# Performance work log

Measured on AMD Instinct MI355X. Metric: run time of the kernel, lower is better.

## Reference

```python
import jax, jax.numpy as jnp
import numpy as np

N, E = 20000, 320000
IN, OUT, H1, H2 = 256, 32, 8, 1
NEG_SLOPE = 0.2


def _gatv2(x, src, dst, Wsrc, bsrc, Wdst, bdst, attn, Wres, bres, heads, dout):
    n = x.shape[0]
    fs = (x @ Wsrc + bsrc).reshape(n, heads, dout)   # (N,H,D)
    fd = (x @ Wdst + bdst).reshape(n, heads, dout)   # (N,H,D)
    # GATv2: leaky_relu BEFORE the attention dot product
    e = jax.nn.leaky_relu(fs[src] + fd[dst], NEG_SLOPE)      # (E,H,D)
    logits = jnp.einsum('ehd,hd->eh', e, attn)               # (E,H)
    # edge softmax over destination-node segments
    m = jax.ops.segment_max(logits, dst, num_segments=n)     # (N,H)
    ex = jnp.exp(logits - m[dst])
    s = jax.ops.segment_sum(ex, dst, num_segments=n)         # (N,H)
    alpha = ex / s[dst]                                      # (E,H)
    msg = alpha[:, :, None] * fs[src]                        # (E,H,D)
    out = jax.ops.segment_sum(msg, dst, num_segments=n)      # (N,H,D)
    res = (x @ Wres + bres).reshape(n, heads, dout)          # residual (dims differ -> Linear)
    return out + res


def setup_inputs() -> dict:
    key = jax.random.key(0)
    ks = jax.random.split(key, 16)
    sc = lambda fin: 1.0 / np.sqrt(fin)
    d = {}
    d['x'] = jax.random.normal(ks[0], (N, IN), jnp.float32)
    d['src'] = jax.random.randint(ks[1], (E,), 0, N, jnp.int32)
    d['dst'] = jax.random.randint(ks[2], (E,), 0, N, jnp.int32)
    # layer 1: IN -> OUT*H1
    d['Wsrc1'] = jax.random.normal(ks[3], (IN, OUT * H1), jnp.float32) * sc(IN)
    d['bsrc1'] = jnp.zeros((OUT * H1,), jnp.float32)
    d['Wdst1'] = jax.random.normal(ks[4], (IN, OUT * H1), jnp.float32) * sc(IN)
    d['bdst1'] = jnp.zeros((OUT * H1,), jnp.float32)
    d['attn1'] = jax.random.normal(ks[5], (H1, OUT), jnp.float32) * sc(OUT)
    d['Wres1'] = jax.random.normal(ks[6], (IN, OUT * H1), jnp.float32) * sc(IN)
    d['bres1'] = jnp.zeros((OUT * H1,), jnp.float32)
    # layer 2: OUT*H1 -> OUT, 1 head
    D2 = OUT * H1
    d['Wsrc2'] = jax.random.normal(ks[7], (D2, OUT * H2), jnp.float32) * sc(D2)
    d['bsrc2'] = jnp.zeros((OUT * H2,), jnp.float32)
    d['Wdst2'] = jax.random.normal(ks[8], (D2, OUT * H2), jnp.float32) * sc(D2)
    d['bdst2'] = jnp.zeros((OUT * H2,), jnp.float32)
    d['attn2'] = jax.random.normal(ks[9], (H2, OUT), jnp.float32) * sc(OUT)
    d['Wres2'] = jax.random.normal(ks[10], (D2, OUT * H2), jnp.float32) * sc(D2)
    d['bres2'] = jnp.zeros((OUT * H2,), jnp.float32)
    return d


def reference(x, src, dst,
              Wsrc1, bsrc1, Wdst1, bdst1, attn1, Wres1, bres1,
              Wsrc2, bsrc2, Wdst2, bdst2, attn2, Wres2, bres2):
    y = _gatv2(x, src, dst, Wsrc1, bsrc1, Wdst1, bdst1, attn1, Wres1, bres1, H1, OUT)
    y = jax.nn.relu(y)                       # (N, 8, OUT)
    y = y.reshape(x.shape[0], -1)            # (N, 8*OUT)
    y = _gatv2(y, src, dst, Wsrc2, bsrc2, Wdst2, bdst2, attn2, Wres2, bres2, H2, OUT)
    return y                                  # (N, 1, OUT)
```

## Files before the change

kernel.cpp:

```cpp
#include <hip/hip_runtime.h>
#include <hip/hip_bf16.h>

#define N_NODES 20000
#define N_PAD   20096
#define N_EDGES 320000
#define D_IN    256
#define NEG     0.2f
#define MAXDEG  64

typedef __attribute__((ext_vector_type(8))) short short8;
typedef __attribute__((ext_vector_type(4))) float f32x4;
typedef __attribute__((ext_vector_type(4))) unsigned short u16x4;

__device__ __forceinline__ unsigned short f2b(float f) {
    unsigned int u = __float_as_uint(f);
    unsigned int r = (u + 0x7FFFu + ((u >> 16) & 1u)) >> 16;
    return (unsigned short)r;
}
__device__ __forceinline__ float b2f(unsigned short u) {
    union { unsigned int i; float f; } v;
    v.i = ((unsigned int)u) << 16;
    return v.f;
}

__device__ __forceinline__ void gload16(const void* g, void* l) {
    __builtin_amdgcn_global_load_lds((const __attribute__((address_space(1))) void*)g,
                                     (__attribute__((address_space(3))) void*)l, 16, 0, 0);
}

#define PB1 2512
#define PB2 3280
#define PB3 3376
#define PB4 3455
#define PREP_BLOCKS 3503
__global__ __launch_bounds__(256) void k_prep(
    const float* __restrict__ x, unsigned short* __restrict__ xb,
    const float* __restrict__ Ws1, const float* __restrict__ Wd1, const float* __restrict__ Wr1,
    unsigned short* __restrict__ wt,
    const float* __restrict__ Ws2, const float* __restrict__ Wd2, const float* __restrict__ Wr2,
    unsigned short* __restrict__ wt2,
    int* __restrict__ cnt, unsigned short* __restrict__ yb)
{
    int bid = blockIdx.x, tid = threadIdx.x;
    if (bid < PB1) {
        int i = bid * 256 + tid;
        int row = i >> 5, c8 = (i & 31) * 8;
        short8 v = {0, 0, 0, 0, 0, 0, 0, 0};
        if (row < N_NODES) {
            float4 a = *reinterpret_cast<const float4*>(x + (size_t)row * 256 + c8);
            float4 b = *reinterpret_cast<const float4*>(x + (size_t)row * 256 + c8 + 4);
            v[0] = (short)f2b(a.x); v[1] = (short)f2b(a.y); v[2] = (short)f2b(a.z); v[3] = (short)f2b(a.w);
            v[4] = (short)f2b(b.x); v[5] = (short)f2b(b.y); v[6] = (short)f2b(b.z); v[7] = (short)f2b(b.w);
        }
        *reinterpret_cast<short8*>(xb + (size_t)row * 256 + c8) = v;
    } else if (bid < PB2) {
        int n = bid - PB1, k = tid;
        const float* W = (n < 256) ? Ws1 : ((n < 512) ? Wd1 : Wr1);
        int c = n & 255;
        wt[(size_t)n * 256 + k] = f2b(W[(size_t)k * 256 + c]);
    } else if (bid < PB3) {
        int n = bid - PB2, k = tid;
        const float* W = (n < 32) ? Ws2 : ((n < 64) ? Wd2 : Wr2);
        int c = n & 31;
        wt2[(size_t)n * 256 + (k ^ ((n & 7) << 3))] = f2b(W[(size_t)k * 32 + c]);
    } else if (bid < PB4) {
        int idx = (bid - PB3) * 256 + tid;
        if (idx < N_NODES) cnt[idx] = 0;
    } else {
        int j = (bid - PB4) * 256 + tid;
        ((unsigned int*)(yb + (size_t)N_NODES * 256))[j] = 0u;
    }
}

#define GEMM1_BLOCKS 942
#define BUCKET_BLOCKS 1250
__global__ __launch_bounds__(256) void k_gemm_l1_mfma(
    const unsigned short* __restrict__ xb,
    const unsigned short* __restrict__ wt,
    const float* __restrict__ bs, const float* __restrict__ bd, const float* __restrict__ br,
    unsigned short* __restrict__ fs, unsigned short* __restrict__ fd, unsigned short* __restrict__ res,
    const int* __restrict__ src, const int* __restrict__ dst,
    int* __restrict__ cnt, int* __restrict__ colp)
{
    __shared__ __align__(16) unsigned short SH[2 * 128 * 64];
    int t = threadIdx.x;
    int bid = blockIdx.x;

    if (bid >= GEMM1_BLOCKS) {
        int e = (bid - GEMM1_BLOCKS) * 256 + t;
        if (e < N_EDGES) {
            int d = dst[e];
            int pos = atomicAdd(&cnt[d], 1);
            if (pos < MAXDEG) colp[d * MAXDEG + pos] = src[e];
        }
        return;
    }

    int lane = t & 63, w = t >> 6;
    const int q = 117, r = 6;
    int xcd = bid & 7, slot = bid >> 3;
    int wg = (xcd < r ? xcd * (q + 1) : r * (q + 1) + (xcd - r) * q) + slot;
    int mb = wg / 6, nb = wg % 6;
    int row0 = mb * 128;
    int which = nb >> 1;
    int col0 = (nb & 1) * 128;
    int ncol0 = nb * 128;
    unsigned short* out = (which == 0) ? fs : ((which == 1) ? fd : res);
    const float* bias   = (which == 0) ? bs : ((which == 1) ? bd : br);
    int wr = w >> 1, wc = w & 1;

    auto stage = [&](int buf, int k0) {
#pragma unroll
        for (int rnd = 0; rnd < 2; rnd++) {
            int c = rnd * 256 + t;
            int row = c >> 2, kc = (c & 3) * 8;
            char* base = (char*)SH + buf * 16384;
            gload16(xb + (size_t)(row0 + row) * 256 + k0 + kc, base + c * 16);
            gload16(wt + (size_t)(ncol0 + row) * 256 + k0 + kc, base + 8192 + c * 16);
        }
    };

    f32x4 acc[4][4] = {};

    stage(0, 0);
    __syncthreads();
    int cur = 0;
#pragma unroll
    for (int it = 0; it < 8; ++it) {
        if (it < 7) stage(cur ^ 1, (it + 1) * 32);
        const char* Ab = (const char*)SH + cur * 16384;
        const char* Bb = Ab + 8192;
        short8 a[4], b[4];
#pragma unroll
        for (int m = 0; m < 4; m++)
            a[m] = *reinterpret_cast<const short8*>(Ab + ((wr * 64 + m * 16 + (lane & 15)) * 64 + (lane >> 4) * 16));
#pragma unroll
        for (int n = 0; n < 4; n++)
            b[n] = *reinterpret_cast<const short8*>(Bb + ((wc * 64 + n * 16 + (lane & 15)) * 64 + (lane >> 4) * 16));
#pragma unroll
        for (int m = 0; m < 4; m++)
#pragma unroll
            for (int n = 0; n < 4; n++)
                acc[m][n] = __builtin_amdgcn_mfma_f32_16x16x32_bf16(a[m], b[n], acc[m][n], 0, 0, 0);
        __syncthreads();
        cur ^= 1;
    }

    int cgrp = lane >> 4, ccol = lane & 15;
    float bvals[4];
#pragma unroll
    for (int n = 0; n < 4; n++) bvals[n] = bias[col0 + wc * 64 + n * 16 + ccol];

#pragma unroll
    for (int p = 0; p < 2; p++) {
        if (p) __syncthreads();
        if (wr == p) {
#pragma unroll
            for (int m = 0; m < 4; m++)
#pragma unroll
                for (int n = 0; n < 4; n++)
#pragma unroll
                    for (int q2 = 0; q2 < 4; q2++) {
                        int lr = m * 16 + cgrp * 4 + q2;
                        int cb = (wc * 64 + n * 16 + ccol) * 2;
                        int addr = lr * 256 + (cb ^ (((lr >> 2) & 3) << 5));
                        *(unsigned short*)((char*)SH + addr) = f2b(acc[m][n][q2] + bvals[n]);
                    }
        }
        __syncthreads();
#pragma unroll
        for (int it = 0; it < 4; it++) {
            int lr = it * 16 + (t >> 4);
            int cb = (t & 15) * 16;
            short8 v = *(const short8*)((const char*)SH + (lr * 256 + (cb ^ (((lr >> 2) & 3) << 5))));
            int gr = row0 + p * 64 + lr;
            if (gr < N_NODES)
                *reinterpret_cast<short8*>(out + (size_t)gr * 256 + col0 + (t & 15) * 8) = v;
        }
    }
}

__global__ __launch_bounds__(64) void k_gather_l1(
    const int* __restrict__ cnt, const int* __restrict__ colp,
    const unsigned short* __restrict__ fs1, const unsigned short* __restrict__ fd1,
    const unsigned short* __restrict__ res1, const float* __restrict__ attn1,
    unsigned short* __restrict__ y)
{
    int n = blockIdx.x;
    int l = threadIdx.x;
    u16x4 fdv4 = *reinterpret_cast<const u16x4*>(fd1 + (size_t)n * 256 + l * 4);
    float fdv[4] = {b2f(fdv4[0]), b2f(fdv4[1]), b2f(fdv4[2]), b2f(fdv4[3])};
    float4 attv = *reinterpret_cast<const float4*>(attn1 + l * 4);
    float att[4] = {attv.x, attv.y, attv.z, attv.w};

    const int* colrow = colp + (size_t)n * MAXDEG;
    int deg = cnt[n];
    if (deg > MAXDEG) deg = MAXDEG;

    float m = -1e30f, s = 0.f;
    float acc[4] = {0.f, 0.f, 0.f, 0.f};
    int c0 = (0 < deg) ? colrow[0] : 0;
    int c1 = (1 < deg) ? colrow[1] : 0;
    u16x4 f0 = *reinterpret_cast<const u16x4*>(fs1 + (size_t)c0 * 256 + l * 4);
    u16x4 f1 = *reinterpret_cast<const u16x4*>(fs1 + (size_t)c1 * 256 + l * 4);
    for (int idx = 0; idx < deg; ++idx) {
        u16x4 fv4 = f0;
        f0 = f1;
        int c2 = (idx + 2 < deg) ? colrow[idx + 2] : 0;
        f1 = *reinterpret_cast<const u16x4*>(fs1 + (size_t)c2 * 256 + l * 4);
        float fv[4] = {b2f(fv4[0]), b2f(fv4[1]), b2f(fv4[2]), b2f(fv4[3])};
        float t0 = fv[0] + fdv[0]; t0 = t0 > 0.f ? t0 : NEG * t0;
        float t1 = fv[1] + fdv[1]; t1 = t1 > 0.f ? t1 : NEG * t1;
        float t2 = fv[2] + fdv[2]; t2 = t2 > 0.f ? t2 : NEG * t2;
        float t3 = fv[3] + fdv[3]; t3 = t3 > 0.f ? t3 : NEG * t3;
        float p = t0 * att[0] + t1 * att[1] + t2 * att[2] + t3 * att[3];
        p += __shfl_xor(p, 1);
        p += __shfl_xor(p, 2);
        p += __shfl_xor(p, 4);
        float mn = fmaxf(m, p);
        float e  = __expf(p - mn);
        float sc = __expf(m - mn);
        s = s * sc + e;
        acc[0] = acc[0] * sc + e * fv[0];
        acc[1] = acc[1] * sc + e * fv[1];
        acc[2] = acc[2] * sc + e * fv[2];
        acc[3] = acc[3] * sc + e * fv[3];
        m = mn;
    }
    u16x4 rv4 = *reinterpret_cast<const u16x4*>(res1 + (size_t)n * 256 + l * 4);
    float inv = (s > 0.f) ? 1.f / s : 0.f;
    u16x4 o;
    o[0] = f2b(fmaxf(acc[0] * inv + b2f(rv4[0]), 0.f));
    o[1] = f2b(fmaxf(acc[1] * inv + b2f(rv4[1]), 0.f));
    o[2] = f2b(fmaxf(acc[2] * inv + b2f(rv4[2]), 0.f));
    o[3] = f2b(fmaxf(acc[3] * inv + b2f(rv4[3]), 0.f));
    *reinterpret_cast<u16x4*>(y + (size_t)n * 256 + l * 4) = o;
}

__global__ __launch_bounds__(256) void k_gemm_l2_mfma(
    const unsigned short* __restrict__ yb,
    const unsigned short* __restrict__ wt2,
    const float* __restrict__ bs, const float* __restrict__ bd, const float* __restrict__ br,
    unsigned short* __restrict__ fs2, unsigned short* __restrict__ fd2, unsigned short* __restrict__ res2)
{
    __shared__ __align__(16) unsigned short Bs[96 * 256];
    __shared__ __align__(16) unsigned short As[2][64 * 32];
    int t = threadIdx.x;
    int lane = t & 63, w = t >> 6;
    int row0 = blockIdx.x * 64;

    auto stage_a = [&](int buf, int k0) {
        int c = t;
        int row = c >> 2, kc = (c & 3) * 8;
        gload16(yb + (size_t)(row0 + row) * 256 + k0 + kc, (char*)As[buf] + c * 16);
    };

#pragma unroll
    for (int i = 0; i < 12; i++) {
        int c = i * 256 + t;
        gload16(wt2 + (size_t)c * 8, (char*)Bs + (size_t)c * 16);
    }
    stage_a(0, 0);
    __syncthreads();

    f32x4 acc[6] = {};
    int arow0 = w * 16;
    int cur = 0;

#pragma unroll
    for (int it = 0; it < 8; ++it) {
        if (it < 7) stage_a(cur ^ 1, (it + 1) * 32);
        short8 a = *reinterpret_cast<const short8*>((const char*)As[cur] + ((arow0 + (lane & 15)) * 64 + (lane >> 4) * 16));
        short8 b[6];
#pragma unroll
        for (int n = 0; n < 6; n++) {
            int brow = n * 16 + (lane & 15);
            int kbyte = (it * 32 + (lane >> 4) * 8) * 2;
            b[n] = *reinterpret_cast<const short8*>((const char*)Bs + (brow * 512 + (kbyte ^ ((brow & 7) << 4))));
        }
#pragma unroll
        for (int n = 0; n < 6; n++)
            acc[n] = __builtin_amdgcn_mfma_f32_16x16x32_bf16(a, b[n], acc[n], 0, 0, 0);
        __syncthreads();
        cur ^= 1;
    }

    int cgrp = lane >> 4, ccol = lane & 15;
#pragma unroll
    for (int n = 0; n < 6; n++) {
        int which = n >> 1;
        int cc = (n & 1) * 16 + ccol;
        unsigned short* out = (which == 0) ? fs2 : ((which == 1) ? fd2 : res2);
        const float* bias   = (which == 0) ? bs  : ((which == 1) ? bd  : br);
        float bv = bias[cc];
        int rbase = row0 + arow0 + cgrp * 4;
#pragma unroll
        for (int q2 = 0; q2 < 4; q2++) {
            int rr = rbase + q2;
            if (rr < N_NODES) out[(size_t)rr * 32 + cc] = f2b(acc[n][q2] + bv);
        }
    }
}

__global__ __launch_bounds__(64) void k_gather_l2(
    const int* __restrict__ cnt, const int* __restrict__ colp,
    const unsigned short* __restrict__ fs2, const unsigned short* __restrict__ fd2,
    const unsigned short* __restrict__ res2, const float* __restrict__ attn2,
    float* __restrict__ out)
{
    int n = blockIdx.x;
    int l = threadIdx.x;
    int d = l & 31, h = l >> 5;
    float fdv = b2f(fd2[(size_t)n * 32 + d]);
    float att = attn2[d];
    const int* colrow = colp + (size_t)n * MAXDEG;
    int deg = cnt[n];
    if (deg > MAXDEG) deg = MAXDEG;

    float m = -1e30f, s = 0.f, acc = 0.f;
    int c0 = (h < deg) ? colrow[h] : 0;
    float fv_next = b2f(fs2[(size_t)c0 * 32 + d]);
    for (int i = h; i < deg; i += 2) {
        float fv = fv_next;
        int cn = (i + 2 < deg) ? colrow[i + 2] : 0;
        fv_next = b2f(fs2[(size_t)cn * 32 + d]);
        float t0 = fv + fdv; t0 = t0 > 0.f ? t0 : NEG * t0;
        float p = t0 * att;
        p += __shfl_xor(p, 1);
        p += __shfl_xor(p, 2);
        p += __shfl_xor(p, 4);
        p += __shfl_xor(p, 8);
        p += __shfl_xor(p, 16);
        float mn = fmaxf(m, p);
        float e  = __expf(p - mn);
        float sc = __expf(m - mn);
        s = s * sc + e;
        acc = acc * sc + e * fv;
        m = mn;
    }
    float mo = __shfl_xor(m, 32);
    float mstar = fmaxf(m, mo);
    float myc = __expf(m - mstar);
    float sp = s * myc, ap = acc * myc;
    float st = sp + __shfl_xor(sp, 32);
    float at = ap + __shfl_xor(ap, 32);
    if (l < 32) {
        float rv = b2f(res2[(size_t)n * 32 + d]);
        float inv = (st > 0.f) ? 1.f / st : 0.f;
        out[(size_t)n * 32 + d] = at * inv + rv;
    }
}

extern "C" void kernel_launch(void* const* d_in, const int* in_sizes, int n_in,
                              void* d_out, int out_size, void* d_ws, size_t ws_size,
                              hipStream_t stream)
{
    const float* x   = (const float*)d_in[0];
    const int*   src = (const int*)d_in[1];
    const int*   dst = (const int*)d_in[2];
    const float* Ws1 = (const float*)d_in[3];
    const float* bs1 = (const float*)d_in[4];
    const float* Wd1 = (const float*)d_in[5];
    const float* bd1 = (const float*)d_in[6];
    const float* at1 = (const float*)d_in[7];
    const float* Wr1 = (const float*)d_in[8];
    const float* br1 = (const float*)d_in[9];
    const float* Ws2 = (const float*)d_in[10];
    const float* bs2 = (const float*)d_in[11];
    const float* Wd2 = (const float*)d_in[12];
    const float* bd2 = (const float*)d_in[13];
    const float* at2 = (const float*)d_in[14];
    const float* Wr2 = (const float*)d_in[15];
    const float* br2 = (const float*)d_in[16];
    float* out = (float*)d_out;

    char* w = (char*)d_ws;
    size_t off = 0;
    auto alloc = [&](size_t bytes) { void* p = w + off; off += (bytes + 255) & ~(size_t)255; return p; };
    int*   cnt    = (int*)  alloc((size_t)N_NODES * 4);
    int*   colp   = (int*)  alloc((size_t)N_NODES * MAXDEG * 4);
    unsigned short* fs1 = (unsigned short*)alloc((size_t)N_NODES * 256 * 2);
    unsigned short* fd1 = (unsigned short*)alloc((size_t)N_NODES * 256 * 2);
    unsigned short* res1= (unsigned short*)alloc((size_t)N_NODES * 256 * 2);
    unsigned short* fs2 = (unsigned short*)alloc((size_t)N_NODES * 32 * 2);
    unsigned short* fd2 = (unsigned short*)alloc((size_t)N_NODES * 32 * 2);
    unsigned short* res2= (unsigned short*)alloc((size_t)N_NODES * 32 * 2);
    unsigned short* xb  = (unsigned short*)alloc((size_t)N_PAD * 256 * 2);
    unsigned short* yb  = (unsigned short*)alloc((size_t)N_PAD * 256 * 2);
    unsigned short* wt  = (unsigned short*)alloc((size_t)768 * 256 * 2);
    unsigned short* wt2 = (unsigned short*)alloc((size_t)96 * 256 * 2);
    (void)ws_size; (void)in_sizes; (void)n_in; (void)out_size;

    k_prep<<<PREP_BLOCKS, 256, 0, stream>>>(x, xb, Ws1, Wd1, Wr1, wt, Ws2, Wd2, Wr2, wt2,
                                            cnt, yb);
    k_gemm_l1_mfma<<<GEMM1_BLOCKS + BUCKET_BLOCKS, 256, 0, stream>>>(
        xb, wt, bs1, bd1, br1, fs1, fd1, res1, src, dst, cnt, colp);
    k_gather_l1<<<N_NODES, 64, 0, stream>>>(cnt, colp, fs1, fd1, res1, at1, yb);
    k_gemm_l2_mfma<<<N_PAD / 64, 256, 0, stream>>>(yb, wt2, bs2, bd2, br2, fs2, fd2, res2);
    k_gather_l2<<<N_NODES, 64, 0, stream>>>(cnt, colp, fs2, fd2, res2, at2, out);
}
```

Measured before the change: 112.6 us.

## Replace global-atomic edge bucketing with multi-pass binned counting sort

Edge bucketing by destination previously used per-edge global atomics on a per-node counter, run inside the layer-1 GEMM launch. It is replaced by a binned counting sort: per-block histograms of dst>>6 built in the prep kernel, a column scan, a scatter into bin-sorted (dst,src) pairs, and a per-bin pass that fills colp with shared-memory atomics. This is meant to cut global atomic contention and scattered writes. The cost is three extra serial launches, an extra 2.5MB intermediate buffer, and the loss of overlap with the GEMM, because bucketing no longer shares its launch.

New measurement: 111.0 us. No clear change (-1.4%).

```diff
diff --git a/kernel.cpp b/kernel.cpp
--- a/kernel.cpp
+++ b/kernel.cpp
@@ -7,6 +7,9 @@
 #define D_IN    256
 #define NEG     0.2f
 #define MAXDEG  64
+#define NSB     64
+#define EPSB    5000
+#define NBIN    313
 
 typedef __attribute__((ext_vector_type(8))) short short8;
 typedef __attribute__((ext_vector_type(4))) float f32x4;
@@ -31,15 +34,16 @@
 #define PB1 2512
 #define PB2 3280
 #define PB3 3376
-#define PB4 3455
-#define PREP_BLOCKS 3503
+#define PB4 3440
+#define PREP_BLOCKS 3488
 __global__ __launch_bounds__(256) void k_prep(
     const float* __restrict__ x, unsigned short* __restrict__ xb,
     const float* __restrict__ Ws1, const float* __restrict__ Wd1, const float* __restrict__ Wr1,
     unsigned short* __restrict__ wt,
     const float* __restrict__ Ws2, const float* __restrict__ Wd2, const float* __restrict__ Wr2,
     unsigned short* __restrict__ wt2,
-    int* __restrict__ cnt, unsigned short* __restrict__ yb)
+    const int* __restrict__ dst, int* __restrict__ blockhist,
+    unsigned short* __restrict__ yb)
 {
     int bid = blockIdx.x, tid = threadIdx.x;
     if (bid < PB1) {
@@ -64,38 +68,105 @@
         int c = n & 31;
         wt2[(size_t)n * 256 + (k ^ ((n & 7) << 3))] = f2b(W[(size_t)k * 32 + c]);
     } else if (bid < PB4) {
-        int idx = (bid - PB3) * 256 + tid;
-        if (idx < N_NODES) cnt[idx] = 0;
+        __shared__ int hist[NBIN];
+        int blk = bid - PB3;
+        for (int b = tid; b < NBIN; b += 256) hist[b] = 0;
+        __syncthreads();
+        for (int it = 0; it < 20; ++it) {
+            int li = it * 256 + tid;
+            if (li < EPSB) atomicAdd(&hist[dst[blk * EPSB + li] >> 6], 1);
+        }
+        __syncthreads();
+        for (int b = tid; b < NBIN; b += 256) blockhist[blk * NBIN + b] = hist[b];
     } else {
         int j = (bid - PB4) * 256 + tid;
         ((unsigned int*)(yb + (size_t)N_NODES * 256))[j] = 0u;
     }
 }
 
+__global__ __launch_bounds__(64) void k_pass2(const int* __restrict__ blockhist,
+                                              int* __restrict__ start, int* __restrict__ bintotal)
+{
+    int bin = blockIdx.x, l = threadIdx.x;
+    int v = blockhist[l * NBIN + bin];
+    int xv = v;
+    for (int off = 1; off < 64; off <<= 1) {
+        int u = __shfl_up(xv, off);
+        if (l >= off) xv += u;
+    }
+    start[l * NBIN + bin] = xv - v;
+    if (l == 63) bintotal[bin] = xv;
+}
+
+__global__ __launch_bounds__(320) void k_pass3(
+    const int* __restrict__ src, const int* __restrict__ dst,
+    const int* __restrict__ start, const int* __restrict__ bintotal,
+    unsigned long long* __restrict__ sorted, int* __restrict__ binbase_g)
+{
+    __shared__ int tmp[320];
+    __shared__ int binbase[NBIN];
+    __shared__ int rank[NBIN];
+    int blk = blockIdx.x, tid = threadIdx.x;
+    int bt = (tid < NBIN) ? bintotal[tid] : 0;
+    tmp[tid] = bt;
+    __syncthreads();
+    for (int off = 1; off < 320; off <<= 1) {
+        int v = (tid >= off) ? tmp[tid - off] : 0;
+        __syncthreads();
+        tmp[tid] += v;
+        __syncthreads();
+    }
+    if (tid < NBIN) {
+        int excl = tmp[tid] - bt;
+        binbase[tid] = excl;
+        rank[tid] = start[blk * NBIN + tid];
+        if (blk == 0) binbase_g[tid] = excl;
+    }
+    __syncthreads();
+    for (int it = 0; it < 16; ++it) {
+        int li = it * 320 + tid;
+        if (li < EPSB) {
+            int e = blk * EPSB + li;
+            int d = dst[e];
+            int b = d >> 6;
+            int r = atomicAdd(&rank[b], 1);
+            sorted[binbase[b] + r] = ((unsigned long long)(unsigned)d << 32) | (unsigned)src[e];
+        }
+    }
+}
+
+__global__ __launch_bounds__(256) void k_pass4(
+    const unsigned long long* __restrict__ sorted,
+    const int* __restrict__ binbase_g, const int* __restrict__ bintotal,
+    int* __restrict__ colp, int* __restrict__ cnt)
+{
+    __shared__ int ch[64];
+    int nb = blockIdx.x, tid = threadIdx.x;
+    if (tid < 64) ch[tid] = 0;
+    __syncthreads();
+    int base = binbase_g[nb], tot = bintotal[nb];
+    for (int i = tid; i < tot; i += 256) {
+        unsigned long long p = sorted[base + i];
+        int d = (int)(p >> 32);
+        int s = (int)(p & 0xffffffffULL);
+        int r = atomicAdd(&ch[d & 63], 1);
+        if (r < MAXDEG) colp[(size_t)d * MAXDEG + r] = s;
+    }
+    __syncthreads();
+    int node = nb * 64 + tid;
+    if (tid < 64 && node < N_NODES) cnt[node] = ch[tid];
+}
+
 #define GEMM1_BLOCKS 942
-#define BUCKET_BLOCKS 1250
 __global__ __launch_bounds__(256) void k_gemm_l1_mfma(
     const unsigned short* __restrict__ xb,
     const unsigned short* __restrict__ wt,
     const float* __restrict__ bs, const float* __restrict__ bd, const float* __restrict__ br,
-    unsigned short* __restrict__ fs, unsigned short* __restrict__ fd, unsigned short* __restrict__ res,
-    const int* __restrict__ src, const int* __restrict__ dst,
-    int* __restrict__ cnt, int* __restrict__ colp)
+    unsigned short* __restrict__ fs, unsigned short* __restrict__ fd, unsigned short* __restrict__ res)
 {
     __shared__ __align__(16) unsigned short SH[2 * 128 * 64];
     int t = threadIdx.x;
     int bid = blockIdx.x;
-
-    if (bid >= GEMM1_BLOCKS) {
-        int e = (bid - GEMM1_BLOCKS) * 256 + t;
-        if (e < N_EDGES) {
-            int d = dst[e];
-            int pos = atomicAdd(&cnt[d], 1);
-            if (pos < MAXDEG) colp[d * MAXDEG + pos] = src[e];
-        }
-        return;
-    }
-
     int lane = t & 63, w = t >> 6;
     const int q = 117, r = 6;
     int xcd = bid & 7, slot = bid >> 3;
@@ -377,8 +448,13 @@
     char* w = (char*)d_ws;
     size_t off = 0;
     auto alloc = [&](size_t bytes) { void* p = w + off; off += (bytes + 255) & ~(size_t)255; return p; };
-    int*   cnt    = (int*)  alloc((size_t)N_NODES * 4);
-    int*   colp   = (int*)  alloc((size_t)N_NODES * MAXDEG * 4);
+    int*   cnt       = (int*)  alloc((size_t)N_NODES * 4);
+    int*   colp      = (int*)  alloc((size_t)N_NODES * MAXDEG * 4);
+    int*   blockhist = (int*)  alloc((size_t)NSB * NBIN * 4);
+    int*   start     = (int*)  alloc((size_t)NSB * NBIN * 4);
+    int*   bintotal  = (int*)  alloc((size_t)NBIN * 4);
+    int*   binbase   = (int*)  alloc((size_t)NBIN * 4);
+    unsigned long long* sorted = (unsigned long long*)alloc((size_t)N_EDGES * 8);
     unsigned short* fs1 = (unsigned short*)alloc((size_t)N_NODES * 256 * 2);
     unsigned short* fd1 = (unsigned short*)alloc((size_t)N_NODES * 256 * 2);
     unsigned short* res1= (unsigned short*)alloc((size_t)N_NODES * 256 * 2);
@@ -392,9 +468,11 @@
     (void)ws_size; (void)in_sizes; (void)n_in; (void)out_size;
 
     k_prep<<<PREP_BLOCKS, 256, 0, stream>>>(x, xb, Ws1, Wd1, Wr1, wt, Ws2, Wd2, Wr2, wt2,
-                                            cnt, yb);
-    k_gemm_l1_mfma<<<GEMM1_BLOCKS + BUCKET_BLOCKS, 256, 0, stream>>>(
-        xb, wt, bs1, bd1, br1, fs1, fd1, res1, src, dst, cnt, colp);
+                                            dst, blockhist, yb);
+    k_pass2<<<NBIN, 64, 0, stream>>>(blockhist, start, bintotal);
+    k_pass3<<<NSB, 320, 0, stream>>>(src, dst, start, bintotal, sorted, binbase);
+    k_pass4<<<NBIN, 256, 0, stream>>>(sorted, binbase, bintotal, colp, cnt);
+    k_gemm_l1_mfma<<<GEMM1_BLOCKS, 256, 0, stream>>>(xb, wt, bs1, bd1, br1, fs1, fd1, res1);
     k_gather_l1<<<N_NODES, 64, 0, stream>>>(cnt, colp, fs1, fd1, res1, at1, yb);
     k_gemm_l2_mfma<<<N_PAD / 64, 256, 0, stream>>>(yb, wt2, bs2, bd2, br2, fs2, fd2, res2);
     k_gather_l2<<<N_NODES, 64, 0, stream>>>(cnt, colp, fs2, fd2, res2, at2, out);
```
